# Kernel optimization log

Measured on AMD Instinct MI355X. Metric: run time of the kernel, lower is better.

## Reference

```python
import jax, jax.numpy as jnp
import numpy as np
import math

# --- static config (matches init_kwargs) ---
NZ, NX, NPAD = 300, 500, 40
DZ = DX = 10.0
DT = 1e-3
NZP, NXP = NZ + NPAD, NX + 2 * NPAD  # freeSurface=True
B, C = 2, 8  # num_vels, num_shots

# --- staggered-grid 4th-order first-derivative stencils (5x5, torch conv2d = cross-correlation) ---
def _kern(taps):
    k = np.zeros((5, 5), np.float32)
    for (r, c), v in taps.items():
        k[r, c] = v
    return jnp.asarray(k).reshape(1, 1, 5, 5)

_a, _b = 1.0 / 24.0, 9.0 / 8.0
KZ  = _kern({(1, 2): _a / DZ, (2, 2): -_b / DZ, (3, 2): _b / DZ, (4, 2): -_a / DZ})
KZU = _kern({(0, 2): _a / DZ, (1, 2): -_b / DZ, (2, 2): _b / DZ, (3, 2): -_a / DZ})
KX  = _kern({(2, 1): _a / DX, (2, 2): -_b / DX, (2, 3): _b / DX, (2, 4): -_a / DX})
KXU = _kern({(2, 0): _a / DX, (2, 1): -_b / DX, (2, 2): _b / DX, (2, 3): -_a / DX})

# --- PML damping profiles (ones in interior, quadratic ramps in pads; overwritten, not multiplied) ---
def _pml():
    vmax, R = 4000.0, 1e-5
    coef = -math.log(R) * 3.0 * vmax / (2.0 * (DX * NPAD) ** 2)
    ax = np.ones((NZP, NXP), np.float64)
    ax[:, :NPAD] = coef * (NPAD - np.arange(NPAD) - 1) ** 2
    ax[:, NX + NPAD:] = coef * np.arange(NPAD) ** 2
    az = np.ones((NZP, NXP), np.float64)  # free surface: top untouched
    az[NZ:NZ + NPAD, :] = (coef * np.arange(NPAD) ** 2)[:, None]
    return (jnp.asarray(ax, jnp.float32)[None, None],
            jnp.asarray(az, jnp.float32)[None, None])

AX, AZ = _pml()

def dconv(x, k):
    # depthwise 'same' 5x5 conv: fold channels into batch, single-channel kernel
    b, c, h, w = x.shape
    y = jax.lax.conv_general_dilated(x.reshape(b * c, 1, h, w), k, (1, 1), ((2, 2), (2, 2)))
    return y.reshape(b, c, h, w)


def setup_inputs() -> dict:
    key = jax.random.key(0)
    ks = iter(jax.random.split(key, 24))
    state_names = ["txx", "tzz", "txz", "vx_x", "vx_z", "vz_x", "vz_z",
                   "txx_x", "txx_z", "tzz_x", "tzz_z", "txz_x", "txz_z"]
    inp = {n: jax.random.normal(next(ks), (B, C, NZP, NXP), jnp.float32) * 0.1 for n in state_names}
    inp["vp"] = jax.random.uniform(next(ks), (B, 1, NZP, NXP), jnp.float32, 1.5, 4.0)
    inp["vs"] = jax.random.uniform(next(ks), (B, 1, NZP, NXP), jnp.float32, 0.8, 2.3)
    inp["rho"] = jax.random.uniform(next(ks), (B, 1, NZP, NXP), jnp.float32, 0.5, 1.5)
    inp["fs"] = jax.random.normal(next(ks), (B,), jnp.float32)
    inp["zs"] = jax.random.randint(next(ks), (C,), 0, NZ)
    inp["xs"] = jax.random.randint(next(ks), (C,), 0, NX)
    return inp


def reference(vp, vs, rho, txx, tzz, txz,
              vx_x, vx_z, vz_x, vz_z,
              txx_x, txx_z, tzz_x, tzz_z, txz_x, txz_z,
              fs, zs, xs):
    dt = DT
    dax = 1.0 - dt * AX  # [1,1,H,W]
    daz = 1.0 - dt * AZ

    # source injection into tzz (freeSurface: z index unpadded, x shifted by npad)
    ch = jnp.arange(C)
    tzz = tzz.at[:, ch, zs, xs + NPAD].add(fs[:, None])

    # velocity update (PML-split)
    var_txx_x = dconv(txx, KX) / rho
    var_txz_z = dconv(txz, KZU) / rho
    var_txz_x = dconv(txz, KXU) / rho
    var_tzz_z = dconv(tzz, KZ) / rho
    vx_x = dax * vx_x + dt * var_txx_x
    vx_z = daz * vx_z + dt * var_txz_z
    vx = vx_x + vx_z
    vz_x = dax * vz_x + dt * var_txz_x
    vz_z = daz * vz_z + dt * var_tzz_z
    vz = vz_x + vz_z

    # stress update (PML-split)
    var_vx_x = dconv(vx, KXU)
    var_vx_z = dconv(vx, KZ)
    var_vz_x = dconv(vz, KX)
    var_vz_z = dconv(vz, KZU)
    lam2mu = vp * vp * rho          # lambda + 2*mu
    lam = lam2mu - 2.0 * vs * vs * rho
    mu = vs * vs * rho
    txx_x = dax * txx_x + dt * lam2mu * var_vx_x
    txx_z = daz * txx_z + dt * lam * var_vz_z
    txx = txx_x + txx_z
    tzz_x = dax * tzz_x + dt * lam * var_vx_x
    tzz_z = daz * tzz_z + dt * lam2mu * var_vz_z
    tzz = tzz_x + tzz_z
    txz_x = dax * txz_x + dt * mu * var_vz_x
    txz_z = daz * txz_z + dt * mu * var_vx_z
    txz = txz_x + txz_z

    return jnp.stack([vx, vz, txx, tzz, txz,
                      vx_x, vx_z, vz_x, vz_z,
                      txx_x, txx_z, tzz_x, tzz_z, txz_x, txz_z])
```

## Files before the change

### kernel.cpp

```cpp
#include <hip/hip_runtime.h>

constexpr int NZ   = 300, NX = 500, NPAD = 40;
constexpr int NZP  = NZ + NPAD;
constexpr int NXP  = NX + 2 * NPAD;
constexpr int Bdim = 2, Cdim = 8;
constexpr int HW   = NZP * NXP;
constexpr int S    = Bdim * Cdim * HW;
constexpr int NQ   = NXP / 4;
constexpr int TQ   = Bdim * Cdim * NZP * NQ;
constexpr float DT = 1e-3f;
constexpr float A2 = (float)((1.0 / 24.0) / 10.0);
constexpr float B2 = (float)((9.0 / 8.0) / 10.0);
constexpr float COEF = 0.43173470493638357f;

typedef float4 f4;

__device__ __forceinline__ f4 ld4(const float* p) { return *reinterpret_cast<const f4*>(p); }
__device__ __forceinline__ void st4(float* p, f4 v) { *reinterpret_cast<f4*>(p) = v; }
__device__ __forceinline__ void unp(float* w, f4 v) { w[0]=v.x; w[1]=v.y; w[2]=v.z; w[3]=v.w; }
__device__ __forceinline__ f4 mk4(const float* a) { return f4{a[0], a[1], a[2], a[3]}; }

__device__ __forceinline__ float dax_of(int j) {
    float ax = 1.0f;
    if (j < NPAD)                { int r = NPAD - 1 - j;      ax = COEF * (float)(r * r); }
    else if (j >= NX + NPAD)     { int r = j - (NX + NPAD);   ax = COEF * (float)(r * r); }
    return 1.0f - DT * ax;
}
__device__ __forceinline__ float daz_of(int i) {
    float az = 1.0f;
    if (i >= NZ)                 { int r = i - NZ;            az = COEF * (float)(r * r); }
    return 1.0f - DT * az;
}

__global__ __launch_bounds__(256) void k_vel(
    const float* __restrict__ txx, const float* __restrict__ tzz, const float* __restrict__ txz,
    const float* __restrict__ vx_x, const float* __restrict__ vx_z,
    const float* __restrict__ vz_x, const float* __restrict__ vz_z,
    const float* __restrict__ rho,
    const float* __restrict__ fs, const int* __restrict__ zs, const int* __restrict__ xs,
    float* __restrict__ out)
{
    int Q = blockIdx.x * 256 + threadIdx.x;
    if (Q >= TQ) return;
    int q  = Q % NQ;
    int t  = Q / NQ;
    int i  = t % NZP;
    int bc = t / NZP;
    int c  = bc % Cdim;
    int b  = bc / Cdim;
    int j0 = q * 4;
    int p  = i * NXP + j0;
    long gidx = (long)bc * HW + p;

    const bool hasL  = (q > 0),        hasR  = (q < NQ - 1);
    const bool hasU1 = (i >= 1),       hasU2 = (i >= 2);
    const bool hasD1 = (i + 1 < NZP),  hasD2 = (i + 2 < NZP);
    const f4 z4 = {0.f, 0.f, 0.f, 0.f};

    const float* TXX = txx + (long)bc * HW;
    const float* TZZ = tzz + (long)bc * HW;
    const float* TXZ = txz + (long)bc * HW;

    float wxx[12];
    unp(wxx,     hasL ? ld4(TXX + p - 4) : z4);
    unp(wxx + 4, ld4(TXX + p));
    unp(wxx + 8, hasR ? ld4(TXX + p + 4) : z4);

    float wxz[12];
    unp(wxz,     hasL ? ld4(TXZ + p - 4) : z4);
    unp(wxz + 4, ld4(TXZ + p));
    unp(wxz + 8, hasR ? ld4(TXZ + p + 4) : z4);
    float zu2[4], zu1[4], zd1[4];
    unp(zu2, hasU2 ? ld4(TXZ + p - 2 * NXP) : z4);
    unp(zu1, hasU1 ? ld4(TXZ + p - NXP)     : z4);
    unp(zd1, hasD1 ? ld4(TXZ + p + NXP)     : z4);

    float tu1[4], t0[4], td1[4], td2[4];
    unp(tu1, hasU1 ? ld4(TZZ + p - NXP)     : z4);
    unp(t0,  ld4(TZZ + p));
    unp(td1, hasD1 ? ld4(TZZ + p + NXP)     : z4);
    unp(td2, hasD2 ? ld4(TZZ + p + 2 * NXP) : z4);
    {
        int sz  = zs[c];
        int sxp = xs[c] + NPAD;
        int e   = sxp - j0;
        if (e >= 0 && e < 4) {
            float fsb = fs[b];
            #pragma unroll
            for (int k = 0; k < 4; ++k) if (k == e) {
                if (i - 1 == sz) tu1[k] += fsb;
                if (i     == sz) t0[k]  += fsb;
                if (i + 1 == sz) td1[k] += fsb;
                if (i + 2 == sz) td2[k] += fsb;
            }
        }
    }

    float rr[4];  unp(rr,  ld4(rho  + (long)b * HW + p));
    float pxx[4]; unp(pxx, ld4(vx_x + gidx));
    float pxz[4]; unp(pxz, ld4(vx_z + gidx));
    float pzx[4]; unp(pzx, ld4(vz_x + gidx));
    float pzz[4]; unp(pzz, ld4(vz_z + gidx));

    float daz = daz_of(i);
    float o_vx[4], o_vz[4], o_vxx[4], o_vxz[4], o_vzx[4], o_vzz[4];
    #pragma unroll
    for (int e = 0; e < 4; ++e) {
        float rinv = 1.0f / rr[e];
        float var_txx_x = (A2 * (wxx[3 + e] - wxx[6 + e]) + B2 * (wxx[5 + e] - wxx[4 + e])) * rinv;
        float var_txz_x = (A2 * (wxz[2 + e] - wxz[5 + e]) + B2 * (wxz[4 + e] - wxz[3 + e])) * rinv;
        float var_txz_z = (A2 * (zu2[e]     - zd1[e])     + B2 * (wxz[4 + e] - zu1[e]))     * rinv;
        float var_tzz_z = (A2 * (tu1[e]     - td2[e])     + B2 * (td1[e]     - t0[e]))      * rinv;
        float dax = dax_of(j0 + e);
        float nvx_x = dax * pxx[e] + DT * var_txx_x;
        float nvx_z = daz * pxz[e] + DT * var_txz_z;
        float nvz_x = dax * pzx[e] + DT * var_txz_x;
        float nvz_z = daz * pzz[e] + DT * var_tzz_z;
        o_vxx[e] = nvx_x; o_vxz[e] = nvx_z; o_vzx[e] = nvz_x; o_vzz[e] = nvz_z;
        o_vx[e] = nvx_x + nvx_z; o_vz[e] = nvz_x + nvz_z;
    }

    st4(out + 0 * (long)S + gidx, mk4(o_vx));
    st4(out + 1 * (long)S + gidx, mk4(o_vz));
    st4(out + 5 * (long)S + gidx, mk4(o_vxx));
    st4(out + 6 * (long)S + gidx, mk4(o_vxz));
    st4(out + 7 * (long)S + gidx, mk4(o_vzx));
    st4(out + 8 * (long)S + gidx, mk4(o_vzz));
}

__global__ __launch_bounds__(256) void k_stress(
    const float* __restrict__ txx_x, const float* __restrict__ txx_z,
    const float* __restrict__ tzz_x, const float* __restrict__ tzz_z,
    const float* __restrict__ txz_x, const float* __restrict__ txz_z,
    const float* __restrict__ vp, const float* __restrict__ vs, const float* __restrict__ rho,
    float* __restrict__ out)
{
    int Q = blockIdx.x * 256 + threadIdx.x;
    if (Q >= TQ) return;
    int q  = Q % NQ;
    int t  = Q / NQ;
    int i  = t % NZP;
    int bc = t / NZP;
    int b  = bc / Cdim;
    int j0 = q * 4;
    int p  = i * NXP + j0;
    long gidx = (long)bc * HW + p;

    const bool hasL  = (q > 0),        hasR  = (q < NQ - 1);
    const bool hasU1 = (i >= 1),       hasU2 = (i >= 2);
    const bool hasD1 = (i + 1 < NZP),  hasD2 = (i + 2 < NZP);
    const f4 z4 = {0.f, 0.f, 0.f, 0.f};

    const float* VX = out + 0 * (long)S + (long)bc * HW;
    const float* VZ = out + 1 * (long)S + (long)bc * HW;

    float wx[12];
    unp(wx,     hasL ? ld4(VX + p - 4) : z4);
    unp(wx + 4, ld4(VX + p));
    unp(wx + 8, hasR ? ld4(VX + p + 4) : z4);
    float xu1[4], xd1[4], xd2[4];
    unp(xu1, hasU1 ? ld4(VX + p - NXP)     : z4);
    unp(xd1, hasD1 ? ld4(VX + p + NXP)     : z4);
    unp(xd2, hasD2 ? ld4(VX + p + 2 * NXP) : z4);

    float wz[12];
    unp(wz,     hasL ? ld4(VZ + p - 4) : z4);
    unp(wz + 4, ld4(VZ + p));
    unp(wz + 8, hasR ? ld4(VZ + p + 4) : z4);
    float zu2[4], zu1[4], zd1[4];
    unp(zu2, hasU2 ? ld4(VZ + p - 2 * NXP) : z4);
    unp(zu1, hasU1 ? ld4(VZ + p - NXP)     : z4);
    unp(zd1, hasD1 ? ld4(VZ + p + NXP)     : z4);

    long mp = (long)b * HW + p;
    float vpv[4], vsv[4], rh[4];
    unp(vpv, ld4(vp + mp));
    unp(vsv, ld4(vs + mp));
    unp(rh,  ld4(rho + mp));

    float pxxx[4], pxxz[4], pzzx[4], pzzz[4], pxzx[4], pxzz[4];
    unp(pxxx, ld4(txx_x + gidx));
    unp(pxxz, ld4(txx_z + gidx));
    unp(pzzx, ld4(tzz_x + gidx));
    unp(pzzz, ld4(tzz_z + gidx));
    unp(pxzx, ld4(txz_x + gidx));
    unp(pxzz, ld4(txz_z + gidx));

    float daz = daz_of(i);
    float o_txx[4], o_tzz[4], o_txz[4];
    float o_xxx[4], o_xxz[4], o_zzx[4], o_zzz[4], o_xzx[4], o_xzz[4];
    #pragma unroll
    for (int e = 0; e < 4; ++e) {
        float var_vx_x = A2 * (wx[2 + e] - wx[5 + e]) + B2 * (wx[4 + e] - wx[3 + e]);
        float var_vx_z = A2 * (xu1[e]    - xd2[e])    + B2 * (xd1[e]    - wx[4 + e]);
        float var_vz_x = A2 * (wz[3 + e] - wz[6 + e]) + B2 * (wz[5 + e] - wz[4 + e]);
        float var_vz_z = A2 * (zu2[e]    - zd1[e])    + B2 * (wz[4 + e] - zu1[e]);

        float lam2mu = vpv[e] * vpv[e] * rh[e];
        float mu     = vsv[e] * vsv[e] * rh[e];
        float lam    = lam2mu - 2.0f * mu;
        float dax = dax_of(j0 + e);

        float ntxx_x = dax * pxxx[e] + DT * lam2mu * var_vx_x;
        float ntxx_z = daz * pxxz[e] + DT * lam    * var_vz_z;
        float ntzz_x = dax * pzzx[e] + DT * lam    * var_vx_x;
        float ntzz_z = daz * pzzz[e] + DT * lam2mu * var_vz_z;
        float ntxz_x = dax * pxzx[e] + DT * mu     * var_vz_x;
        float ntxz_z = daz * pxzz[e] + DT * mu     * var_vx_z;

        o_txx[e] = ntxx_x + ntxx_z;
        o_tzz[e] = ntzz_x + ntzz_z;
        o_txz[e] = ntxz_x + ntxz_z;
        o_xxx[e] = ntxx_x; o_xxz[e] = ntxx_z;
        o_zzx[e] = ntzz_x; o_zzz[e] = ntzz_z;
        o_xzx[e] = ntxz_x; o_xzz[e] = ntxz_z;
    }

    st4(out +  2 * (long)S + gidx, mk4(o_txx));
    st4(out +  3 * (long)S + gidx, mk4(o_tzz));
    st4(out +  4 * (long)S + gidx, mk4(o_txz));
    st4(out +  9 * (long)S + gidx, mk4(o_xxx));
    st4(out + 10 * (long)S + gidx, mk4(o_xxz));
    st4(out + 11 * (long)S + gidx, mk4(o_zzx));
    st4(out + 12 * (long)S + gidx, mk4(o_zzz));
    st4(out + 13 * (long)S + gidx, mk4(o_xzx));
    st4(out + 14 * (long)S + gidx, mk4(o_xzz));
}

extern "C" void kernel_launch(void* const* d_in, const int* in_sizes, int n_in,
                              void* d_out, int out_size, void* d_ws, size_t ws_size,
                              hipStream_t stream) {
    const float* txx   = (const float*)d_in[0];
    const float* tzz   = (const float*)d_in[1];
    const float* txz   = (const float*)d_in[2];
    const float* vx_x  = (const float*)d_in[3];
    const float* vx_z  = (const float*)d_in[4];
    const float* vz_x  = (const float*)d_in[5];
    const float* vz_z  = (const float*)d_in[6];
    const float* txx_x = (const float*)d_in[7];
    const float* txx_z = (const float*)d_in[8];
    const float* tzz_x = (const float*)d_in[9];
    const float* tzz_z = (const float*)d_in[10];
    const float* txz_x = (const float*)d_in[11];
    const float* txz_z = (const float*)d_in[12];
    const float* vp    = (const float*)d_in[13];
    const float* vs    = (const float*)d_in[14];
    const float* rho   = (const float*)d_in[15];
    const float* fs    = (const float*)d_in[16];
    const int*   zs    = (const int*)d_in[17];
    const int*   xs    = (const int*)d_in[18];
    float* out = (float*)d_out;

    dim3 grid((TQ + 255) / 256), block(256);
    k_vel<<<grid, block, 0, stream>>>(txx, tzz, txz, vx_x, vx_z, vz_x, vz_z,
                                      rho, fs, zs, xs, out);
    k_stress<<<grid, block, 0, stream>>>(txx_x, txx_z, tzz_x, tzz_z, txz_x, txz_z,
                                         vp, vs, rho, out);
}
```

Before: 344.2 us.

## Register-block 4 rows per thread with vertical ring buffers and nontemporal stores

Each thread now walks a 4-row vertical segment of one 4-column strip. It keeps a sliding ring of the z-stencil rows in registers, so the vertical neighbours are loaded once and reused instead of being re-fetched per row. The thread mapping is reordered so consecutive threads cover adjacent columns within a segment. Nontemporal stores are used for outputs not re-read by the next kernel, keeping the vx/vz outputs cached for the stress kernel. The risks are fewer threads (less parallelism and occupancy), higher register pressure, and possible cache-policy side effects of the nontemporal stores.

```diff
diff --git a/kernel.cpp b/kernel.cpp
--- a/kernel.cpp
+++ b/kernel.cpp
@@ -7,16 +7,24 @@
 constexpr int HW   = NZP * NXP;
 constexpr int S    = Bdim * Cdim * HW;
 constexpr int NQ   = NXP / 4;
-constexpr int TQ   = Bdim * Cdim * NZP * NQ;
+constexpr int COLS = Bdim * Cdim * NQ;
+constexpr int LSEG = 4;
+constexpr int NSEG = NZP / LSEG;
+constexpr int TT   = COLS * NSEG;
 constexpr float DT = 1e-3f;
 constexpr float A2 = (float)((1.0 / 24.0) / 10.0);
 constexpr float B2 = (float)((9.0 / 8.0) / 10.0);
 constexpr float COEF = 0.43173470493638357f;
 
 typedef float4 f4;
+typedef float nf4 __attribute__((ext_vector_type(4)));
 
 __device__ __forceinline__ f4 ld4(const float* p) { return *reinterpret_cast<const f4*>(p); }
 __device__ __forceinline__ void st4(float* p, f4 v) { *reinterpret_cast<f4*>(p) = v; }
+__device__ __forceinline__ void stnt4(float* p, f4 v) {
+    nf4 w; w.x = v.x; w.y = v.y; w.z = v.z; w.w = v.w;
+    __builtin_nontemporal_store(w, reinterpret_cast<nf4*>(p));
+}
 __device__ __forceinline__ void unp(float* w, f4 v) { w[0]=v.x; w[1]=v.y; w[2]=v.z; w[3]=v.w; }
 __device__ __forceinline__ f4 mk4(const float* a) { return f4{a[0], a[1], a[2], a[3]}; }
 
@@ -40,92 +48,114 @@
     const float* __restrict__ fs, const int* __restrict__ zs, const int* __restrict__ xs,
     float* __restrict__ out)
 {
-    int Q = blockIdx.x * 256 + threadIdx.x;
-    if (Q >= TQ) return;
-    int q  = Q % NQ;
-    int t  = Q / NQ;
-    int i  = t % NZP;
-    int bc = t / NZP;
-    int c  = bc % Cdim;
-    int b  = bc / Cdim;
-    int j0 = q * 4;
-    int p  = i * NXP + j0;
-    long gidx = (long)bc * HW + p;
-
-    const bool hasL  = (q > 0),        hasR  = (q < NQ - 1);
-    const bool hasU1 = (i >= 1),       hasU2 = (i >= 2);
-    const bool hasD1 = (i + 1 < NZP),  hasD2 = (i + 2 < NZP);
-    const f4 z4 = {0.f, 0.f, 0.f, 0.f};
+    int t = blockIdx.x * 256 + threadIdx.x;
+    if (t >= TT) return;
+    int col = t % COLS;
+    int seg = t / COLS;
+    int q   = col % NQ;
+    int bc  = col / NQ;
+    int c   = bc % Cdim;
+    int b   = bc / Cdim;
+    int j0  = q * 4;
+    int z0  = seg * LSEG;
 
     const float* TXX = txx + (long)bc * HW;
     const float* TZZ = tzz + (long)bc * HW;
     const float* TXZ = txz + (long)bc * HW;
-
-    float wxx[12];
-    unp(wxx,     hasL ? ld4(TXX + p - 4) : z4);
-    unp(wxx + 4, ld4(TXX + p));
-    unp(wxx + 8, hasR ? ld4(TXX + p + 4) : z4);
-
-    float wxz[12];
-    unp(wxz,     hasL ? ld4(TXZ + p - 4) : z4);
-    unp(wxz + 4, ld4(TXZ + p));
-    unp(wxz + 8, hasR ? ld4(TXZ + p + 4) : z4);
-    float zu2[4], zu1[4], zd1[4];
-    unp(zu2, hasU2 ? ld4(TXZ + p - 2 * NXP) : z4);
-    unp(zu1, hasU1 ? ld4(TXZ + p - NXP)     : z4);
-    unp(zd1, hasD1 ? ld4(TXZ + p + NXP)     : z4);
-
-    float tu1[4], t0[4], td1[4], td2[4];
-    unp(tu1, hasU1 ? ld4(TZZ + p - NXP)     : z4);
-    unp(t0,  ld4(TZZ + p));
-    unp(td1, hasD1 ? ld4(TZZ + p + NXP)     : z4);
-    unp(td2, hasD2 ? ld4(TZZ + p + 2 * NXP) : z4);
-    {
-        int sz  = zs[c];
-        int sxp = xs[c] + NPAD;
-        int e   = sxp - j0;
-        if (e >= 0 && e < 4) {
-            float fsb = fs[b];
+    const float* RHO = rho + (long)b * HW;
+    const bool hasL = (q > 0), hasR = (q < NQ - 1);
+    const f4 z4 = {0.f, 0.f, 0.f, 0.f};
+
+    int sz  = zs[c];
+    int e_inj = xs[c] + NPAD - j0;
+    float fsb = fs[b];
+    const bool inj = (e_inj >= 0 && e_inj < 4);
+
+    auto ldC = [&](const float* F, int r) -> f4 {
+        return (r >= 0 && r < NZP) ? ld4(F + r * NXP + j0) : z4;
+    };
+
+    float ringX[4][4], ringZ[4][4];
+    #pragma unroll
+    for (int k = 0; k < 4; ++k) {
+        unp(ringX[k], ldC(TXZ, z0 - 2 + k));
+        float tmp[4]; unp(tmp, ldC(TZZ, z0 - 1 + k));
+        if (inj && (z0 - 1 + k) == sz) {
             #pragma unroll
-            for (int k = 0; k < 4; ++k) if (k == e) {
-                if (i - 1 == sz) tu1[k] += fsb;
-                if (i     == sz) t0[k]  += fsb;
-                if (i + 1 == sz) td1[k] += fsb;
-                if (i + 2 == sz) td2[k] += fsb;
+            for (int m = 0; m < 4; ++m) if (m == e_inj) tmp[m] += fsb;
+        }
+        #pragma unroll
+        for (int m = 0; m < 4; ++m) ringZ[k][m] = tmp[m];
+    }
+
+    float dax0[4];
+    #pragma unroll
+    for (int m = 0; m < 4; ++m) dax0[m] = dax_of(j0 + m);
+
+    #pragma unroll
+    for (int rr = 0; rr < LSEG; ++rr) {
+        int r = z0 + rr;
+        int p = r * NXP + j0;
+        long gidx = (long)bc * HW + p;
+
+        float wxx[12];
+        unp(wxx,     hasL ? ld4(TXX + p - 4) : z4);
+        unp(wxx + 4, ld4(TXX + p));
+        unp(wxx + 8, hasR ? ld4(TXX + p + 4) : z4);
+
+        float wxz[12];
+        unp(wxz,     hasL ? ld4(TXZ + p - 4) : z4);
+        #pragma unroll
+        for (int m = 0; m < 4; ++m) wxz[4 + m] = ringX[(rr + 2) & 3][m];
+        unp(wxz + 8, hasR ? ld4(TXZ + p + 4) : z4);
+
+        float rr4[4]; unp(rr4, ld4(RHO + p));
+        float pxx[4], pxz[4], pzx[4], pzz[4];
+        unp(pxx, ld4(vx_x + gidx));
+        unp(pxz, ld4(vx_z + gidx));
+        unp(pzx, ld4(vz_x + gidx));
+        unp(pzz, ld4(vz_z + gidx));
+
+        float daz = daz_of(r);
+        float ovx[4], ovz[4], ovxx[4], ovxz[4], ovzx[4], ovzz[4];
+        #pragma unroll
+        for (int m = 0; m < 4; ++m) {
+            float rinv = 1.0f / rr4[m];
+            float var_txx_x = (A2 * (wxx[3 + m] - wxx[6 + m]) + B2 * (wxx[5 + m] - wxx[4 + m])) * rinv;
+            float var_txz_x = (A2 * (wxz[2 + m] - wxz[5 + m]) + B2 * (wxz[4 + m] - wxz[3 + m])) * rinv;
+            float txz_im2 = ringX[(rr) & 3][m], txz_im1 = ringX[(rr + 1) & 3][m];
+            float txz_0   = ringX[(rr + 2) & 3][m], txz_ip1 = ringX[(rr + 3) & 3][m];
+            float tzz_im1 = ringZ[(rr) & 3][m], tzz_0   = ringZ[(rr + 1) & 3][m];
+            float tzz_ip1 = ringZ[(rr + 2) & 3][m], tzz_ip2 = ringZ[(rr + 3) & 3][m];
+            float var_txz_z = (A2 * (txz_im2 - txz_ip1) + B2 * (txz_0   - txz_im1)) * rinv;
+            float var_tzz_z = (A2 * (tzz_im1 - tzz_ip2) + B2 * (tzz_ip1 - tzz_0  )) * rinv;
+
+            float nvx_x = dax0[m] * pxx[m] + DT * var_txx_x;
+            float nvx_z = daz     * pxz[m] + DT * var_txz_z;
+            float nvz_x = dax0[m] * pzx[m] + DT * var_txz_x;
+            float nvz_z = daz     * pzz[m] + DT * var_tzz_z;
+            ovxx[m] = nvx_x; ovxz[m] = nvx_z; ovzx[m] = nvz_x; ovzz[m] = nvz_z;
+            ovx[m] = nvx_x + nvx_z; ovz[m] = nvz_x + nvz_z;
+        }
+
+        st4  (out + 0 * (long)S + gidx, mk4(ovx));
+        st4  (out + 1 * (long)S + gidx, mk4(ovz));
+        stnt4(out + 5 * (long)S + gidx, mk4(ovxx));
+        stnt4(out + 6 * (long)S + gidx, mk4(ovxz));
+        stnt4(out + 7 * (long)S + gidx, mk4(ovzx));
+        stnt4(out + 8 * (long)S + gidx, mk4(ovzz));
+
+        if (rr < LSEG - 1) {
+            unp(ringX[rr & 3], ldC(TXZ, r + 2));
+            float tmp[4]; unp(tmp, ldC(TZZ, r + 3));
+            if (inj && (r + 3) == sz) {
+                #pragma unroll
+                for (int m = 0; m < 4; ++m) if (m == e_inj) tmp[m] += fsb;
             }
+            #pragma unroll
+            for (int m = 0; m < 4; ++m) ringZ[rr & 3][m] = tmp[m];
         }
     }
-
-    float rr[4];  unp(rr,  ld4(rho  + (long)b * HW + p));
-    float pxx[4]; unp(pxx, ld4(vx_x + gidx));
-    float pxz[4]; unp(pxz, ld4(vx_z + gidx));
-    float pzx[4]; unp(pzx, ld4(vz_x + gidx));
-    float pzz[4]; unp(pzz, ld4(vz_z + gidx));
-
-    float daz = daz_of(i);
-    float o_vx[4], o_vz[4], o_vxx[4], o_vxz[4], o_vzx[4], o_vzz[4];
-    #pragma unroll
-    for (int e = 0; e < 4; ++e) {
-        float rinv = 1.0f / rr[e];
-        float var_txx_x = (A2 * (wxx[3 + e] - wxx[6 + e]) + B2 * (wxx[5 + e] - wxx[4 + e])) * rinv;
-        float var_txz_x = (A2 * (wxz[2 + e] - wxz[5 + e]) + B2 * (wxz[4 + e] - wxz[3 + e])) * rinv;
-        float var_txz_z = (A2 * (zu2[e]     - zd1[e])     + B2 * (wxz[4 + e] - zu1[e]))     * rinv;
-        float var_tzz_z = (A2 * (tu1[e]     - td2[e])     + B2 * (td1[e]     - t0[e]))      * rinv;
-        float dax = dax_of(j0 + e);
-        float nvx_x = dax * pxx[e] + DT * var_txx_x;
-        float nvx_z = daz * pxz[e] + DT * var_txz_z;
-        float nvz_x = dax * pzx[e] + DT * var_txz_x;
-        float nvz_z = daz * pzz[e] + DT * var_tzz_z;
-        o_vxx[e] = nvx_x; o_vxz[e] = nvx_z; o_vzx[e] = nvz_x; o_vzz[e] = nvz_z;
-        o_vx[e] = nvx_x + nvx_z; o_vz[e] = nvz_x + nvz_z;
-    }
-
-    st4(out + 0 * (long)S + gidx, mk4(o_vx));
-    st4(out + 1 * (long)S + gidx, mk4(o_vz));
-    st4(out + 5 * (long)S + gidx, mk4(o_vxx));
-    st4(out + 6 * (long)S + gidx, mk4(o_vxz));
-    st4(out + 7 * (long)S + gidx, mk4(o_vzx));
-    st4(out + 8 * (long)S + gidx, mk4(o_vzz));
 }
 
 __global__ __launch_bounds__(256) void k_stress(
@@ -135,96 +165,116 @@
     const float* __restrict__ vp, const float* __restrict__ vs, const float* __restrict__ rho,
     float* __restrict__ out)
 {
-    int Q = blockIdx.x * 256 + threadIdx.x;
-    if (Q >= TQ) return;
-    int q  = Q % NQ;
-    int t  = Q / NQ;
-    int i  = t % NZP;
-    int bc = t / NZP;
-    int b  = bc / Cdim;
-    int j0 = q * 4;
-    int p  = i * NXP + j0;
-    long gidx = (long)bc * HW + p;
-
-    const bool hasL  = (q > 0),        hasR  = (q < NQ - 1);
-    const bool hasU1 = (i >= 1),       hasU2 = (i >= 2);
-    const bool hasD1 = (i + 1 < NZP),  hasD2 = (i + 2 < NZP);
-    const f4 z4 = {0.f, 0.f, 0.f, 0.f};
+    int t = blockIdx.x * 256 + threadIdx.x;
+    if (t >= TT) return;
+    int col = t % COLS;
+    int seg = t / COLS;
+    int q   = col % NQ;
+    int bc  = col / NQ;
+    int b   = bc / Cdim;
+    int j0  = q * 4;
+    int z0  = seg * LSEG;
 
     const float* VX = out + 0 * (long)S + (long)bc * HW;
     const float* VZ = out + 1 * (long)S + (long)bc * HW;
-
-    float wx[12];
-    unp(wx,     hasL ? ld4(VX + p - 4) : z4);
-    unp(wx + 4, ld4(VX + p));
-    unp(wx + 8, hasR ? ld4(VX + p + 4) : z4);
-    float xu1[4], xd1[4], xd2[4];
-    unp(xu1, hasU1 ? ld4(VX + p - NXP)     : z4);
-    unp(xd1, hasD1 ? ld4(VX + p + NXP)     : z4);
-    unp(xd2, hasD2 ? ld4(VX + p + 2 * NXP) : z4);
-
-    float wz[12];
-    unp(wz,     hasL ? ld4(VZ + p - 4) : z4);
-    unp(wz + 4, ld4(VZ + p));
-    unp(wz + 8, hasR ? ld4(VZ + p + 4) : z4);
-    float zu2[4], zu1[4], zd1[4];
-    unp(zu2, hasU2 ? ld4(VZ + p - 2 * NXP) : z4);
-    unp(zu1, hasU1 ? ld4(VZ + p - NXP)     : z4);
-    unp(zd1, hasD1 ? ld4(VZ + p + NXP)     : z4);
-
-    long mp = (long)b * HW + p;
-    float vpv[4], vsv[4], rh[4];
-    unp(vpv, ld4(vp + mp));
-    unp(vsv, ld4(vs + mp));
-    unp(rh,  ld4(rho + mp));
-
-    float pxxx[4], pxxz[4], pzzx[4], pzzz[4], pxzx[4], pxzz[4];
-    unp(pxxx, ld4(txx_x + gidx));
-    unp(pxxz, ld4(txx_z + gidx));
-    unp(pzzx, ld4(tzz_x + gidx));
-    unp(pzzz, ld4(tzz_z + gidx));
-    unp(pxzx, ld4(txz_x + gidx));
-    unp(pxzz, ld4(txz_z + gidx));
-
-    float daz = daz_of(i);
-    float o_txx[4], o_tzz[4], o_txz[4];
-    float o_xxx[4], o_xxz[4], o_zzx[4], o_zzz[4], o_xzx[4], o_xzz[4];
-    #pragma unroll
-    for (int e = 0; e < 4; ++e) {
-        float var_vx_x = A2 * (wx[2 + e] - wx[5 + e]) + B2 * (wx[4 + e] - wx[3 + e]);
-        float var_vx_z = A2 * (xu1[e]    - xd2[e])    + B2 * (xd1[e]    - wx[4 + e]);
-        float var_vz_x = A2 * (wz[3 + e] - wz[6 + e]) + B2 * (wz[5 + e] - wz[4 + e]);
-        float var_vz_z = A2 * (zu2[e]    - zd1[e])    + B2 * (wz[4 + e] - zu1[e]);
-
-        float lam2mu = vpv[e] * vpv[e] * rh[e];
-        float mu     = vsv[e] * vsv[e] * rh[e];
-        float lam    = lam2mu - 2.0f * mu;
-        float dax = dax_of(j0 + e);
-
-        float ntxx_x = dax * pxxx[e] + DT * lam2mu * var_vx_x;
-        float ntxx_z = daz * pxxz[e] + DT * lam    * var_vz_z;
-        float ntzz_x = dax * pzzx[e] + DT * lam    * var_vx_x;
-        float ntzz_z = daz * pzzz[e] + DT * lam2mu * var_vz_z;
-        float ntxz_x = dax * pxzx[e] + DT * mu     * var_vz_x;
-        float ntxz_z = daz * pxzz[e] + DT * mu     * var_vx_z;
-
-        o_txx[e] = ntxx_x + ntxx_z;
-        o_tzz[e] = ntzz_x + ntzz_z;
-        o_txz[e] = ntxz_x + ntxz_z;
-        o_xxx[e] = ntxx_x; o_xxz[e] = ntxx_z;
-        o_zzx[e] = ntzz_x; o_zzz[e] = ntzz_z;
-        o_xzx[e] = ntxz_x; o_xzz[e] = ntxz_z;
+    const bool hasL = (q > 0), hasR = (q < NQ - 1);
+    const f4 z4 = {0.f, 0.f, 0.f, 0.f};
+
+    auto ldC = [&](const float* F, int r) -> f4 {
+        return (r >= 0 && r < NZP) ? ld4(F + r * NXP + j0) : z4;
+    };
+
+    float ringVX[4][4], ringVZ[4][4];
+    #pragma unroll
+    for (int k = 0; k < 4; ++k) {
+        unp(ringVX[k], ldC(VX, z0 - 1 + k));
+        unp(ringVZ[k], ldC(VZ, z0 - 2 + k));
     }
 
-    st4(out +  2 * (long)S + gidx, mk4(o_txx));
-    st4(out +  3 * (long)S + gidx, mk4(o_tzz));
-    st4(out +  4 * (long)S + gidx, mk4(o_txz));
-    st4(out +  9 * (long)S + gidx, mk4(o_xxx));
-    st4(out + 10 * (long)S + gidx, mk4(o_xxz));
-    st4(out + 11 * (long)S + gidx, mk4(o_zzx));
-    st4(out + 12 * (long)S + gidx, mk4(o_zzz));
-    st4(out + 13 * (long)S + gidx, mk4(o_xzx));
-    st4(out + 14 * (long)S + gidx, mk4(o_xzz));
+    float dax0[4];
+    #pragma unroll
+    for (int m = 0; m < 4; ++m) dax0[m] = dax_of(j0 + m);
+
+    #pragma unroll
+    for (int rr = 0; rr < LSEG; ++rr) {
+        int r = z0 + rr;
+        int p = r * NXP + j0;
+        long gidx = (long)bc * HW + p;
+
+        float wvx[12];
+        unp(wvx,     hasL ? ld4(VX + p - 4) : z4);
+        #pragma unroll
+        for (int m = 0; m < 4; ++m) wvx[4 + m] = ringVX[(rr + 1) & 3][m];
+        unp(wvx + 8, hasR ? ld4(VX + p + 4) : z4);
+
+        float wvz[12];
+        unp(wvz,     hasL ? ld4(VZ + p - 4) : z4);
+        #pragma unroll
+        for (int m = 0; m < 4; ++m) wvz[4 + m] = ringVZ[(rr + 2) & 3][m];
+        unp(wvz + 8, hasR ? ld4(VZ + p + 4) : z4);
+
+        long mp = (long)b * HW + p;
+        float vpv[4], vsv[4], rh[4];
+        unp(vpv, ld4(vp + mp));
+        unp(vsv, ld4(vs + mp));
+        unp(rh,  ld4(rho + mp));
+
+        float pxxx[4], pxxz[4], pzzx[4], pzzz[4], pxzx[4], pxzz[4];
+        unp(pxxx, ld4(txx_x + gidx));
+        unp(pxxz, ld4(txx_z + gidx));
+        unp(pzzx, ld4(tzz_x + gidx));
+        unp(pzzz, ld4(tzz_z + gidx));
+        unp(pxzx, ld4(txz_x + gidx));
+        unp(pxzz, ld4(txz_z + gidx));
+
+        float daz = daz_of(r);
+        float o_txx[4], o_tzz[4], o_txz[4];
+        float o_xxx[4], o_xxz[4], o_zzx[4], o_zzz[4], o_xzx[4], o_xzz[4];
+        #pragma unroll
+        for (int m = 0; m < 4; ++m) {
+            float var_vx_x = A2 * (wvx[2 + m] - wvx[5 + m]) + B2 * (wvx[4 + m] - wvx[3 + m]);
+            float var_vz_x = A2 * (wvz[3 + m] - wvz[6 + m]) + B2 * (wvz[5 + m] - wvz[4 + m]);
+            float vx_im1 = ringVX[(rr) & 3][m],     vx_0   = ringVX[(rr + 1) & 3][m];
+            float vx_ip1 = ringVX[(rr + 2) & 3][m], vx_ip2 = ringVX[(rr + 3) & 3][m];
+            float vz_im2 = ringVZ[(rr) & 3][m],     vz_im1 = ringVZ[(rr + 1) & 3][m];
+            float vz_0   = ringVZ[(rr + 2) & 3][m], vz_ip1 = ringVZ[(rr + 3) & 3][m];
+            float var_vx_z = A2 * (vx_im1 - vx_ip2) + B2 * (vx_ip1 - vx_0  );
+            float var_vz_z = A2 * (vz_im2 - vz_ip1) + B2 * (vz_0   - vz_im1);
+
+            float lam2mu = vpv[m] * vpv[m] * rh[m];
+            float mu     = vsv[m] * vsv[m] * rh[m];
+            float lam    = lam2mu - 2.0f * mu;
+
+            float ntxx_x = dax0[m] * pxxx[m] + DT * lam2mu * var_vx_x;
+            float ntxx_z = daz     * pxxz[m] + DT * lam    * var_vz_z;
+            float ntzz_x = dax0[m] * pzzx[m] + DT * lam    * var_vx_x;
+            float ntzz_z = daz     * pzzz[m] + DT * lam2mu * var_vz_z;
+            float ntxz_x = dax0[m] * pxzx[m] + DT * mu     * var_vz_x;
+            float ntxz_z = daz     * pxzz[m] + DT * mu     * var_vx_z;
+
+            o_txx[m] = ntxx_x + ntxx_z;
+            o_tzz[m] = ntzz_x + ntzz_z;
+            o_txz[m] = ntxz_x + ntxz_z;
+            o_xxx[m] = ntxx_x; o_xxz[m] = ntxx_z;
+            o_zzx[m] = ntzz_x; o_zzz[m] = ntzz_z;
+            o_xzx[m] = ntxz_x; o_xzz[m] = ntxz_z;
+        }
+
+        stnt4(out +  2 * (long)S + gidx, mk4(o_txx));
+        stnt4(out +  3 * (long)S + gidx, mk4(o_tzz));
+        stnt4(out +  4 * (long)S + gidx, mk4(o_txz));
+        stnt4(out +  9 * (long)S + gidx, mk4(o_xxx));
+        stnt4(out + 10 * (long)S + gidx, mk4(o_xxz));
+        stnt4(out + 11 * (long)S + gidx, mk4(o_zzx));
+        stnt4(out + 12 * (long)S + gidx, mk4(o_zzz));
+        stnt4(out + 13 * (long)S + gidx, mk4(o_xzx));
+        stnt4(out + 14 * (long)S + gidx, mk4(o_xzz));
+
+        if (rr < LSEG - 1) {
+            unp(ringVX[rr & 3], ldC(VX, r + 3));
+            unp(ringVZ[rr & 3], ldC(VZ, r + 2));
+        }
+    }
 }
 
 extern "C" void kernel_launch(void* const* d_in, const int* in_sizes, int n_in,
@@ -251,7 +301,7 @@
     const int*   xs    = (const int*)d_in[18];
     float* out = (float*)d_out;
 
-    dim3 grid((TQ + 255) / 256), block(256);
+    dim3 grid((TT + 255) / 256), block(256);
     k_vel<<<grid, block, 0, stream>>>(txx, tzz, txz, vx_x, vx_z, vz_x, vz_z,
                                       rho, fs, zs, xs, out);
     k_stress<<<grid, block, 0, stream>>>(txx_x, txx_z, tzz_x, tzz_z, txz_x, txz_z,
```

Result: slower. 380.7 us (+10.6%).
